# Optimization experiments

Hardware: AMD Instinct MI355X
Metric: run time of the kernel (lower is better)

The kernel has to match this reference:

```python
import jax, jax.numpy as jnp
import numpy as np

N_AGENTS = 32
STATE_DIM = 2048
EMBED = 64
BS, T = 64, 32


def setup_inputs() -> dict:
    key = jax.random.key(0)
    ks = jax.random.split(key, 12)
    def lin(k, fan_in, fan_out):
        return jax.random.normal(k, (fan_in, fan_out), dtype=jnp.float32) / np.sqrt(fan_in)
    return {
        "agent_qs": jax.random.normal(ks[0], (BS, T, N_AGENTS), dtype=jnp.float32),
        "states": jax.random.normal(ks[1], (BS, T, STATE_DIM), dtype=jnp.float32),
        "Ww1": lin(ks[2], STATE_DIM, EMBED * N_AGENTS),
        "bw1": jnp.zeros((EMBED * N_AGENTS,), jnp.float32),
        "Wwf": lin(ks[3], STATE_DIM, EMBED),
        "bwf": jnp.zeros((EMBED,), jnp.float32),
        "Wb1": lin(ks[4], STATE_DIM, EMBED),
        "bb1": jnp.zeros((EMBED,), jnp.float32),
        "Wv1": lin(ks[5], STATE_DIM, EMBED),
        "bv1": jnp.zeros((EMBED,), jnp.float32),
        "Wv2": lin(ks[6], EMBED, 1),
        "bv2": jnp.zeros((1,), jnp.float32),
    }


def _mix(qs, st, Ww1, bw1, Wwf, bwf, Wb1, bb1, Wv1, bv1, Wv2, bv2):
    # qs: [B,1,A], st: [B,S] -> q_tot [B]
    w1 = jnp.abs(st @ Ww1 + bw1).reshape(-1, N_AGENTS, EMBED)          # [B,A,E]
    b1 = (st @ Wb1 + bb1)[:, None, :]                                   # [B,1,E]
    hidden = jax.nn.elu(jnp.einsum('bia,bae->bie', qs, w1) + b1)        # [B,1,E]
    w_final = jnp.abs(st @ Wwf + bwf)                                   # [B,E]
    v = jax.nn.relu(st @ Wv1 + bv1) @ Wv2 + bv2                         # [B,1]
    y = jnp.einsum('bie,be->bi', hidden, w_final) + v                   # [B,1]
    return y[:, 0]


def reference(agent_qs, states, Ww1, bw1, Wwf, bwf, Wb1, bb1, Wv1, bv1, Wv2, bv2):
    bs = agent_qs.shape[0]
    st = states.reshape(-1, STATE_DIM)                   # [B,S]
    qs = agent_qs.reshape(-1, 1, N_AGENTS)               # [B,1,A]
    B = st.shape[0]
    params = (Ww1, bw1, Wwf, bwf, Wb1, bb1, Wv1, bv1, Wv2, bv2)

    # --- wc_calculate (fully detached) ---
    q_tot = _mix(qs, st, *params)                        # [B]
    dim2 = STATE_DIM // N_AGENTS
    st3 = st.reshape(B, N_AGENTS, dim2)
    mask = 1.0 - jnp.eye(N_AGENTS, dtype=st.dtype)       # [A,A]: row i zeros agent-i chunk
    masked = (st3[None, :, :, :] * mask[:, None, :, None]).reshape(N_AGENTS * B, STATE_DIM)
    qs_rep = jnp.broadcast_to(qs[None], (N_AGENTS, B, 1, N_AGENTS)).reshape(N_AGENTS * B, 1, N_AGENTS)
    q1 = _mix(qs_rep, masked, *params).reshape(N_AGENTS, B)
    wc = jnp.abs(q_tot[None, :] - q1).T                  # [B,A]
    wc = wc / jnp.maximum(jnp.linalg.norm(wc, axis=1, keepdims=True), 1e-12)
    wc = jax.lax.stop_gradient(wc)[:, None, :]           # [B,1,A]

    # --- final mix with importance-weighted qs ---
    q_tot_final = _mix(qs * wc, st, *params)             # [B]
    return q_tot_final.reshape(bs, -1, 1)
```

## Files before the change

kernel.cpp:

```cpp
#include <hip/hip_runtime.h>
#include <math.h>
#include <stdint.h>

#define NA 32
#define SD 2048
#define BT 2048
#define NFRG 144

typedef float floatx4 __attribute__((ext_vector_type(4)));
typedef short bf16x8  __attribute__((ext_vector_type(8)));

__device__ __forceinline__ unsigned short f2bf(float f) {
    union { float f; uint32_t u; } v; v.f = f;
    uint32_t r = v.u + 0x7FFFu + ((v.u >> 16) & 1u);
    return (unsigned short)(r >> 16);
}


__global__ __launch_bounds__(256) void k0_ast(const float* __restrict__ st,
                                              unsigned short* __restrict__ stA) {
    const int t  = threadIdx.x;
    const int kc = blockIdx.x * 4 + (t >> 6);
    const int bt = blockIdx.y;
    const int l  = t & 63;
    const int quad = l >> 4, l16 = l & 15;
    const float* src = st + (size_t)(bt * 16 + l16) * SD + kc * 32 + quad * 8;
    float4 v0 = *(const float4*)(src);
    float4 v1 = *(const float4*)(src + 4);
    ushort4 o0, o1;
    o0.x = f2bf(v0.x); o0.y = f2bf(v0.y); o0.z = f2bf(v0.z); o0.w = f2bf(v0.w);
    o1.x = f2bf(v1.x); o1.y = f2bf(v1.y); o1.z = f2bf(v1.z); o1.w = f2bf(v1.w);
    unsigned short* dst = stA + ((size_t)bt * 64 + kc) * 512 + l * 8;
    *(ushort4*)(dst)     = o0;
    *(ushort4*)(dst + 4) = o1;
}

__global__ __launch_bounds__(256) void k0_wswz(const float* __restrict__ Ww1,
                                               const float* __restrict__ Wwf,
                                               const float* __restrict__ Wb1,
                                               const float* __restrict__ Wv1,
                                               unsigned short* __restrict__ Wswz) {
    const int t = threadIdx.x;
    const int i = blockIdx.y;
    const int f = blockIdx.x * 2 + (t >> 7);
    const int h = (t >> 6) & 1;
    const int l = t & 63;
    const int quad = l >> 4, l16 = l & 15;
    const int n = f * 16 + l16;

    const float* src; int ld, nr = 0;
    if (f < 128)      { src = Ww1; ld = 2048; nr = n; }
    else if (f < 132) { src = Wwf; ld = 64;   nr = n - 2048; }
    else if (f < 136) { src = Wb1; ld = 64;   nr = n - 2112; }
    else if (f < 140) { src = Wv1; ld = 64;   nr = n - 2176; }
    else              { src = nullptr; ld = 64; }

    const int k0 = i * 64 + h * 32 + quad * 8;
    unsigned short vals[8];
    #pragma unroll
    for (int j = 0; j < 8; j++)
        vals[j] = src ? f2bf(src[(size_t)(k0 + j) * ld + nr]) : (unsigned short)0;

    unsigned short* dst = Wswz + (((size_t)i * NFRG + f) * 2 + h) * 512 + l * 8;
    ushort4 o0 = {vals[0], vals[1], vals[2], vals[3]};
    ushort4 o1 = {vals[4], vals[5], vals[6], vals[7]};
    *(ushort4*)(dst)     = o0;
    *(ushort4*)(dst + 4) = o1;
}

__global__ void k0_bias(const float* __restrict__ bw1, const float* __restrict__ bwf,
                        const float* __restrict__ bb1, const float* __restrict__ bv1,
                        float* __restrict__ bcat) {
    int n = blockIdx.x * 256 + threadIdx.x;
    if (n >= NFRG * 16) return;
    float v = 0.f;
    if (n < 2048)      v = bw1[n];
    else if (n < 2112) v = bwf[n - 2048];
    else if (n < 2176) v = bb1[n - 2112];
    else if (n < 2240) v = bv1[n - 2176];
    bcat[n] = v;
}

__global__ __launch_bounds__(256) void k1_gemm(const unsigned short* __restrict__ stA,
                                               const unsigned short* __restrict__ Wswz,
                                               const float* __restrict__ bcat,
                                               float* __restrict__ Ycn)
{
    const int t = threadIdx.x;
    const int m0t = blockIdx.x * 4;
    const int n0f = blockIdx.y * 8;
    const int wid = t >> 6, lane = t & 63;
    const int wm = wid & 1, wn = wid >> 1;
    const int l16 = lane & 15;

    floatx4 acc[2][4];
    #pragma unroll
    for (int i = 0; i < 2; i++)
        #pragma unroll
        for (int j = 0; j < 4; j++) acc[i][j] = (floatx4)0.f;

    const unsigned short* Ap0 = stA + ((size_t)(m0t + wm * 2 + 0) * 64) * 512 + lane * 8;
    const unsigned short* Ap1 = stA + ((size_t)(m0t + wm * 2 + 1) * 64) * 512 + lane * 8;
    const unsigned short* Bbase = Wswz + ((size_t)(n0f + wn * 4) * 2) * 512 + lane * 8;

    bf16x8 a0c = *(const bf16x8*)(Ap0);
    bf16x8 a1c = *(const bf16x8*)(Ap1);
    bf16x8 bc[4];
    #pragma unroll
    for (int nf = 0; nf < 4; nf++)
        bc[nf] = *(const bf16x8*)(Bbase + (size_t)nf * 1024);

    for (int kc = 0; kc < 64; kc++) {
        bf16x8 a0n, a1n, bn[4];
        if (kc < 63) {
            const int kn = kc + 1;
            a0n = *(const bf16x8*)(Ap0 + (size_t)kn * 512);
            a1n = *(const bf16x8*)(Ap1 + (size_t)kn * 512);
            const unsigned short* Bp =
                Bbase + ((size_t)(kn >> 1) * NFRG * 2 + (kn & 1)) * 512;
            #pragma unroll
            for (int nf = 0; nf < 4; nf++)
                bn[nf] = *(const bf16x8*)(Bp + (size_t)nf * 1024);
        }
        #pragma unroll
        for (int nf = 0; nf < 4; nf++) {
            acc[0][nf] = __builtin_amdgcn_mfma_f32_16x16x32_bf16(a0c, bc[nf], acc[0][nf], 0, 0, 0);
            acc[1][nf] = __builtin_amdgcn_mfma_f32_16x16x32_bf16(a1c, bc[nf], acc[1][nf], 0, 0, 0);
        }
        a0c = a0n; a1c = a1n;
        #pragma unroll
        for (int nf = 0; nf < 4; nf++) bc[nf] = bn[nf];
    }

    #pragma unroll
    for (int mf = 0; mf < 2; mf++)
        #pragma unroll
        for (int nf = 0; nf < 4; nf++) {
            const int f  = n0f + wn * 4 + nf;
            const int bt = m0t + wm * 2 + mf;
            const float bias = bcat[f * 16 + l16];
            floatx4 o;
            #pragma unroll
            for (int r = 0; r < 4; r++) o[r] = -(acc[mf][nf][r] + bias);
            *(floatx4*)(Ycn + ((size_t)bt * NFRG + f) * 256 + lane * 4) = o;
        }
}

__global__ __launch_bounds__(64) void k3_q1(
    const unsigned short* __restrict__ stA, const float* __restrict__ qs,
    const unsigned short* __restrict__ Wswz, const float* __restrict__ Wv2,
    const float* __restrict__ bv2, const float* __restrict__ Ycn,
    float* __restrict__ q1)
{
    const int i  = blockIdx.x;
    const int bt = blockIdx.y;
    __shared__ float qs_s[16][33];

    const int t = threadIdx.x;
    const int quad = t >> 4, l16 = t & 15;

    {
        int b = t >> 2, a0 = (t & 3) * 8;
        const float* src = qs + (size_t)(bt * 16 + b) * NA + a0;
        #pragma unroll
        for (int u = 0; u < 8; u++) qs_s[b][a0 + u] = src[u];
    }
    bf16x8 A0 = *(const bf16x8*)(stA + ((size_t)bt * 64 + 2 * i + 0) * 512 + t * 8);
    bf16x8 A1 = *(const bf16x8*)(stA + ((size_t)bt * 64 + 2 * i + 1) * 512 + t * 8);
    __syncthreads();

    floatx4 hid[4];
    #pragma unroll
    for (int nf = 0; nf < 4; nf++) hid[nf] = (floatx4)0.f;

    const float*          Yb = Ycn  + (size_t)bt * NFRG * 256;
    const unsigned short* Wb = Wswz + (size_t)i * NFRG * 1024;

    bf16x8 wc_[8];
    {
        const unsigned short* wp = Wb + t * 8;
        #pragma unroll
        for (int nf = 0; nf < 4; nf++) {
            wc_[nf * 2 + 0] = *(const bf16x8*)(wp + (size_t)nf * 1024);
            wc_[nf * 2 + 1] = *(const bf16x8*)(wp + (size_t)nf * 1024 + 512);
        }
    }

    for (int a = 0; a < 32; a++) {
        bf16x8 wn_[8];
        if (a < 31) {
            const unsigned short* wp = Wb + (size_t)((a + 1) * 4) * 1024 + t * 8;
            #pragma unroll
            for (int nf = 0; nf < 4; nf++) {
                wn_[nf * 2 + 0] = *(const bf16x8*)(wp + (size_t)nf * 1024);
                wn_[nf * 2 + 1] = *(const bf16x8*)(wp + (size_t)nf * 1024 + 512);
            }
        }
        const float* yp = Yb + (size_t)(a * 4) * 256 + t * 4;
        floatx4 acc[4];
        #pragma unroll
        for (int nf = 0; nf < 4; nf++) acc[nf] = *(const floatx4*)(yp + nf * 256);
        #pragma unroll
        for (int nf = 0; nf < 4; nf++) {
            acc[nf] = __builtin_amdgcn_mfma_f32_16x16x32_bf16(A0, wc_[nf*2+0], acc[nf], 0, 0, 0);
            acc[nf] = __builtin_amdgcn_mfma_f32_16x16x32_bf16(A1, wc_[nf*2+1], acc[nf], 0, 0, 0);
        }
        float qv[4];
        #pragma unroll
        for (int r = 0; r < 4; r++) qv[r] = qs_s[quad * 4 + r][a];
        #pragma unroll
        for (int nf = 0; nf < 4; nf++)
            #pragma unroll
            for (int r = 0; r < 4; r++)
                hid[nf][r] += qv[r] * fabsf(acc[nf][r]);
        #pragma unroll
        for (int u = 0; u < 8; u++) wc_[u] = wn_[u];
    }

    floatx4 wff[4], b1f[4], vacc = (floatx4)0.f;
    #pragma unroll
    for (int nft = 0; nft < 12; nft++) {
        const int f = 128 + nft;
        floatx4 c = *(const floatx4*)(Yb + (size_t)f * 256 + t * 4);
        const unsigned short* wp = Wb + (size_t)f * 1024 + t * 8;
        c = __builtin_amdgcn_mfma_f32_16x16x32_bf16(A0, *(const bf16x8*)(wp),       c, 0, 0, 0);
        c = __builtin_amdgcn_mfma_f32_16x16x32_bf16(A1, *(const bf16x8*)(wp + 512), c, 0, 0, 0);
        if (nft < 4) {
            #pragma unroll
            for (int r = 0; r < 4; r++) wff[nft][r] = fabsf(c[r]);
        } else if (nft < 8) {
            #pragma unroll
            for (int r = 0; r < 4; r++) b1f[nft - 4][r] = -c[r];
        } else {
            float wv2 = Wv2[(nft - 8) * 16 + l16];
            #pragma unroll
            for (int r = 0; r < 4; r++) vacc[r] += fmaxf(-c[r], 0.f) * wv2;
        }
    }

    const float bv2v = bv2[0];
    #pragma unroll
    for (int r = 0; r < 4; r++) {
        float s = vacc[r];
        #pragma unroll
        for (int nf = 0; nf < 4; nf++) {
            float h = hid[nf][r] + b1f[nf][r];
            h = h > 0.f ? h : expm1f(h);
            s += h * wff[nf][r];
        }
        s += __shfl_xor(s, 1); s += __shfl_xor(s, 2);
        s += __shfl_xor(s, 4); s += __shfl_xor(s, 8);
        if (l16 == 0) q1[(size_t)i * BT + bt * 16 + quad * 4 + r] = s + bv2v;
    }
}

__global__ __launch_bounds__(256) void k4_final(
    const float* __restrict__ qs, const float* __restrict__ Ycn,
    const float* __restrict__ q1, const float* __restrict__ Wv2,
    const float* __restrict__ bv2, float* __restrict__ out)
{
    const int bt = blockIdx.x;
    __shared__ float qs_s[16][33];
    __shared__ float qw_s[16][33];
    __shared__ float hidp[4][16][64];
    __shared__ float wfb[16][64], b1b[16][64], vb[16][64];
    __shared__ float qt[16];

    const int t = threadIdx.x, w = t >> 6, lane = t & 63;
    const int quad = lane >> 4, l16 = lane & 15;
    const float bv2v = bv2[0];

    {
        int l = t * 2;
        float2 v = *(const float2*)&qs[(size_t)(bt * 16 + (l >> 5)) * NA + (l & 31)];
        qs_s[l >> 5][(l & 31) + 0] = v.x;
        qs_s[l >> 5][(l & 31) + 1] = v.y;
    }
    __syncthreads();

    const float* Yb = Ycn + (size_t)bt * NFRG * 256;

    floatx4 hid[4];
    #pragma unroll
    for (int nf = 0; nf < 4; nf++) hid[nf] = (floatx4)0.f;
    for (int ia = 0; ia < 8; ia++) {
        const int a = w * 8 + ia;
        const float* yp = Yb + (size_t)(a * 4) * 256 + lane * 4;
        float qv[4];
        #pragma unroll
        for (int r = 0; r < 4; r++) qv[r] = qs_s[quad * 4 + r][a];
        #pragma unroll
        for (int nf = 0; nf < 4; nf++) {
            floatx4 c = *(const floatx4*)(yp + nf * 256);
            #pragma unroll
            for (int r = 0; r < 4; r++) hid[nf][r] += qv[r] * fabsf(c[r]);
        }
    }
    #pragma unroll
    for (int nf = 0; nf < 4; nf++)
        #pragma unroll
        for (int r = 0; r < 4; r++)
            hidp[w][quad * 4 + r][nf * 16 + l16] = hid[nf][r];

    #pragma unroll
    for (int fi = 0; fi < 3; fi++) {
        const int nft = w * 3 + fi;
        floatx4 c = *(const floatx4*)(Yb + (size_t)(128 + nft) * 256 + lane * 4);
        const int e = (nft & 3) * 16 + l16;
        #pragma unroll
        for (int r = 0; r < 4; r++) {
            int b = quad * 4 + r;
            if (nft < 4)      wfb[b][e] = fabsf(c[r]);
            else if (nft < 8) b1b[b][e] = -c[r];
            else              vb[b][e]  = fmaxf(-c[r], 0.f) * Wv2[e];
        }
    }
    __syncthreads();

    #pragma unroll
    for (int bb = 0; bb < 4; bb++) {
        int b = w * 4 + bb;
        float h = hidp[0][b][lane] + hidp[1][b][lane]
                + hidp[2][b][lane] + hidp[3][b][lane] + b1b[b][lane];
        h = h > 0.f ? h : expm1f(h);
        float val = h * wfb[b][lane] + vb[b][lane];
        #pragma unroll
        for (int off = 32; off > 0; off >>= 1) val += __shfl_xor(val, off);
        if (lane == 0) qt[b] = val + bv2v;
    }
    __syncthreads();

    {
        const int rr = w * 4 + quad;
        float qtv = qt[rr];
        float d0 = fabsf(qtv - q1[(size_t)(2 * l16 + 0) * BT + bt * 16 + rr]);
        float d1 = fabsf(qtv - q1[(size_t)(2 * l16 + 1) * BT + bt * 16 + rr]);
        float ss = d0 * d0 + d1 * d1;
        ss += __shfl_xor(ss, 1); ss += __shfl_xor(ss, 2);
        ss += __shfl_xor(ss, 4); ss += __shfl_xor(ss, 8);
        float inv = 1.f / fmaxf(sqrtf(ss), 1e-12f);
        qw_s[rr][2 * l16 + 0] = qs_s[rr][2 * l16 + 0] * d0 * inv;
        qw_s[rr][2 * l16 + 1] = qs_s[rr][2 * l16 + 1] * d1 * inv;
    }
    __syncthreads();

    floatx4 hid2[4];
    #pragma unroll
    for (int nf = 0; nf < 4; nf++) hid2[nf] = (floatx4)0.f;
    for (int ia = 0; ia < 8; ia++) {
        const int a = w * 8 + ia;
        const float* yp = Yb + (size_t)(a * 4) * 256 + lane * 4;
        float qv[4];
        #pragma unroll
        for (int r = 0; r < 4; r++) qv[r] = qw_s[quad * 4 + r][a];
        #pragma unroll
        for (int nf = 0; nf < 4; nf++) {
            floatx4 c = *(const floatx4*)(yp + nf * 256);
            #pragma unroll
            for (int r = 0; r < 4; r++) hid2[nf][r] += qv[r] * fabsf(c[r]);
        }
    }
    #pragma unroll
    for (int nf = 0; nf < 4; nf++)
        #pragma unroll
        for (int r = 0; r < 4; r++)
            hidp[w][quad * 4 + r][nf * 16 + l16] = hid2[nf][r];
    __syncthreads();

    #pragma unroll
    for (int bb = 0; bb < 4; bb++) {
        int b = w * 4 + bb;
        float h = hidp[0][b][lane] + hidp[1][b][lane]
                + hidp[2][b][lane] + hidp[3][b][lane] + b1b[b][lane];
        h = h > 0.f ? h : expm1f(h);
        float val = h * wfb[b][lane] + vb[b][lane];
        #pragma unroll
        for (int off = 32; off > 0; off >>= 1) val += __shfl_xor(val, off);
        if (lane == 0) out[bt * 16 + b] = val + bv2v;
    }
}

extern "C" void kernel_launch(void* const* d_in, const int* in_sizes, int n_in,
                              void* d_out, int out_size, void* d_ws, size_t ws_size,
                              hipStream_t stream) {
    const float* qs  = (const float*)d_in[0];
    const float* st  = (const float*)d_in[1];
    const float* Ww1 = (const float*)d_in[2];
    const float* bw1 = (const float*)d_in[3];
    const float* Wwf = (const float*)d_in[4];
    const float* bwf = (const float*)d_in[5];
    const float* Wb1 = (const float*)d_in[6];
    const float* bb1 = (const float*)d_in[7];
    const float* Wv1 = (const float*)d_in[8];
    const float* bv1 = (const float*)d_in[9];
    const float* Wv2 = (const float*)d_in[10];
    const float* bv2 = (const float*)d_in[11];
    float* out = (float*)d_out;

    float* Ycn           = (float*)d_ws;
    unsigned short* stA  = (unsigned short*)(Ycn + (size_t)128 * NFRG * 256);
    unsigned short* Wswz = stA + (size_t)SD * SD;
    float* bcat          = (float*)(Wswz + (size_t)32 * NFRG * 1024);
    float* q1v           = bcat + NFRG * 16;

    k0_ast <<<dim3(16, 128), 256, 0, stream>>>(st, stA);
    k0_wswz<<<dim3(NFRG / 2, 32), 256, 0, stream>>>(Ww1, Wwf, Wb1, Wv1, Wswz);
    k0_bias<<<(NFRG * 16 + 255) / 256, 256, 0, stream>>>(bw1, bwf, bb1, bv1, bcat);

    k1_gemm<<<dim3(BT / 64, NFRG / 8), 256, 0, stream>>>(stA, Wswz, bcat, Ycn);
    k3_q1  <<<dim3(NA, BT / 16), 64, 0, stream>>>(stA, qs, Wswz, Wv2, bv2, Ycn, q1v);
    k4_final<<<BT / 16, 256, 0, stream>>>(qs, Ycn, q1v, Wv2, bv2, out);
}
```

Measured before the change: 215.4 us.

## Restructure q1 kernel: 4-wave blocks sharing LDS-staged weights, two agents per wave

The masked-agent correction kernel now runs 256-thread blocks. Each wave handles one 16-row batch tile and two masked agents (p and p+16), and the four waves share weight fragments that are double-buffered in LDS through global_load_lds. The Ycn bias fragments are loaded once per tile and reused across both agents. This cuts redundant global weight and Ycn traffic per MFMA and overlaps the next fragment's load with compute. In exchange it adds per-iteration block barriers and more register pressure from the doubled accumulators.

```diff
diff --git a/kernel.cpp b/kernel.cpp
--- a/kernel.cpp
+++ b/kernel.cpp
@@ -14,6 +14,13 @@
     union { float f; uint32_t u; } v; v.f = f;
     uint32_t r = v.u + 0x7FFFu + ((v.u >> 16) & 1u);
     return (unsigned short)(r >> 16);
+}
+
+__device__ __forceinline__ void stage16(const void* g, void* l) {
+    __builtin_amdgcn_global_load_lds(
+        (const __attribute__((address_space(1))) void*)g,
+        (__attribute__((address_space(3))) void*)l,
+        16, 0, 0);
 }
 
 
@@ -146,112 +153,171 @@
         }
 }
 
-__global__ __launch_bounds__(64) void k3_q1(
+__global__ __launch_bounds__(256) void k3_q1(
     const unsigned short* __restrict__ stA, const float* __restrict__ qs,
     const unsigned short* __restrict__ Wswz, const float* __restrict__ Wv2,
     const float* __restrict__ bv2, const float* __restrict__ Ycn,
     float* __restrict__ q1)
 {
-    const int i  = blockIdx.x;
-    const int bt = blockIdx.y;
-    __shared__ float qs_s[16][33];
-
+    const int p   = blockIdx.x;
+    const int btg = blockIdx.y;
     const int t = threadIdx.x;
-    const int quad = t >> 4, l16 = t & 15;
-
-    {
-        int b = t >> 2, a0 = (t & 3) * 8;
+    const int w = t >> 6, lane = t & 63;
+    const int bt = btg * 4 + w;
+    const int quad = lane >> 4, l16 = lane & 15;
+    const int im[2] = { p, p + 16 };
+
+    __shared__ unsigned short Wl[2][2][4][2][512];
+    __shared__ float qs_s[4][16][33];
+
+    {
+        int b = lane >> 2, a0 = (lane & 3) * 8;
         const float* src = qs + (size_t)(bt * 16 + b) * NA + a0;
         #pragma unroll
-        for (int u = 0; u < 8; u++) qs_s[b][a0 + u] = src[u];
-    }
-    bf16x8 A0 = *(const bf16x8*)(stA + ((size_t)bt * 64 + 2 * i + 0) * 512 + t * 8);
-    bf16x8 A1 = *(const bf16x8*)(stA + ((size_t)bt * 64 + 2 * i + 1) * 512 + t * 8);
-    __syncthreads();
-
-    floatx4 hid[4];
-    #pragma unroll
-    for (int nf = 0; nf < 4; nf++) hid[nf] = (floatx4)0.f;
-
-    const float*          Yb = Ycn  + (size_t)bt * NFRG * 256;
-    const unsigned short* Wb = Wswz + (size_t)i * NFRG * 1024;
-
-    bf16x8 wc_[8];
-    {
-        const unsigned short* wp = Wb + t * 8;
-        #pragma unroll
-        for (int nf = 0; nf < 4; nf++) {
-            wc_[nf * 2 + 0] = *(const bf16x8*)(wp + (size_t)nf * 1024);
-            wc_[nf * 2 + 1] = *(const bf16x8*)(wp + (size_t)nf * 1024 + 512);
-        }
-    }
-
-    for (int a = 0; a < 32; a++) {
-        bf16x8 wn_[8];
-        if (a < 31) {
-            const unsigned short* wp = Wb + (size_t)((a + 1) * 4) * 1024 + t * 8;
+        for (int u = 0; u < 8; u++) qs_s[w][b][a0 + u] = src[u];
+    }
+
+    bf16x8 A0[2], A1[2];
+    #pragma unroll
+    for (int m = 0; m < 2; m++) {
+        A0[m] = *(const bf16x8*)(stA + ((size_t)bt * 64 + 2 * im[m] + 0) * 512 + lane * 8);
+        A1[m] = *(const bf16x8*)(stA + ((size_t)bt * 64 + 2 * im[m] + 1) * 512 + lane * 8);
+    }
+
+    const float* Yb = Ycn + (size_t)bt * NFRG * 256 + lane * 4;
+
+    auto stage = [&](int fg, int buf) {
+        #pragma unroll
+        for (int j = 0; j < 4; j++) {
+            const int c  = w * 4 + j;
+            const int m  = c >> 3;
+            const int nf = (c >> 1) & 3;
+            const int h  = c & 1;
+            const unsigned short* g = Wswz
+                + ((size_t)(im[m] * NFRG + fg * 4 + nf) * 2 + h) * 512 + lane * 8;
+            stage16(g, &Wl[buf][m][nf][h][0]);
+        }
+    };
+
+    floatx4 yv[4], yn[4], acc[2][4];
+
+    auto wmfma = [&](int buf) {
+        #pragma unroll
+        for (int m = 0; m < 2; m++)
             #pragma unroll
             for (int nf = 0; nf < 4; nf++) {
-                wn_[nf * 2 + 0] = *(const bf16x8*)(wp + (size_t)nf * 1024);
-                wn_[nf * 2 + 1] = *(const bf16x8*)(wp + (size_t)nf * 1024 + 512);
+                bf16x8 w0 = *(const bf16x8*)&Wl[buf][m][nf][0][lane * 8];
+                bf16x8 w1 = *(const bf16x8*)&Wl[buf][m][nf][1][lane * 8];
+                floatx4 a = __builtin_amdgcn_mfma_f32_16x16x32_bf16(A0[m], w0, yv[nf], 0, 0, 0);
+                acc[m][nf] = __builtin_amdgcn_mfma_f32_16x16x32_bf16(A1[m], w1, a, 0, 0, 0);
             }
-        }
-        const float* yp = Yb + (size_t)(a * 4) * 256 + t * 4;
-        floatx4 acc[4];
-        #pragma unroll
-        for (int nf = 0; nf < 4; nf++) acc[nf] = *(const floatx4*)(yp + nf * 256);
-        #pragma unroll
-        for (int nf = 0; nf < 4; nf++) {
-            acc[nf] = __builtin_amdgcn_mfma_f32_16x16x32_bf16(A0, wc_[nf*2+0], acc[nf], 0, 0, 0);
-            acc[nf] = __builtin_amdgcn_mfma_f32_16x16x32_bf16(A1, wc_[nf*2+1], acc[nf], 0, 0, 0);
-        }
+    };
+
+    floatx4 hid[2][4];
+    #pragma unroll
+    for (int m = 0; m < 2; m++)
+        #pragma unroll
+        for (int nf = 0; nf < 4; nf++) hid[m][nf] = (floatx4)0.f;
+
+    stage(0, 0);
+    #pragma unroll
+    for (int nf = 0; nf < 4; nf++) yv[nf] = *(const floatx4*)(Yb + (size_t)nf * 256);
+    __syncthreads();
+
+    for (int fg = 0; fg < 32; fg++) {
+        const int cur = fg & 1;
+        stage(fg + 1, cur ^ 1);
+        {
+            const float* yp = Yb + (size_t)(fg + 1) * 4 * 256;
+            #pragma unroll
+            for (int nf = 0; nf < 4; nf++) yn[nf] = *(const floatx4*)(yp + (size_t)nf * 256);
+        }
+        wmfma(cur);
         float qv[4];
         #pragma unroll
-        for (int r = 0; r < 4; r++) qv[r] = qs_s[quad * 4 + r][a];
-        #pragma unroll
-        for (int nf = 0; nf < 4; nf++)
-            #pragma unroll
-            for (int r = 0; r < 4; r++)
-                hid[nf][r] += qv[r] * fabsf(acc[nf][r]);
-        #pragma unroll
-        for (int u = 0; u < 8; u++) wc_[u] = wn_[u];
-    }
-
-    floatx4 wff[4], b1f[4], vacc = (floatx4)0.f;
-    #pragma unroll
-    for (int nft = 0; nft < 12; nft++) {
-        const int f = 128 + nft;
-        floatx4 c = *(const floatx4*)(Yb + (size_t)f * 256 + t * 4);
-        const unsigned short* wp = Wb + (size_t)f * 1024 + t * 8;
-        c = __builtin_amdgcn_mfma_f32_16x16x32_bf16(A0, *(const bf16x8*)(wp),       c, 0, 0, 0);
-        c = __builtin_amdgcn_mfma_f32_16x16x32_bf16(A1, *(const bf16x8*)(wp + 512), c, 0, 0, 0);
-        if (nft < 4) {
-            #pragma unroll
-            for (int r = 0; r < 4; r++) wff[nft][r] = fabsf(c[r]);
-        } else if (nft < 8) {
-            #pragma unroll
-            for (int r = 0; r < 4; r++) b1f[nft - 4][r] = -c[r];
-        } else {
-            float wv2 = Wv2[(nft - 8) * 16 + l16];
-            #pragma unroll
-            for (int r = 0; r < 4; r++) vacc[r] += fmaxf(-c[r], 0.f) * wv2;
+        for (int r = 0; r < 4; r++) qv[r] = qs_s[w][quad * 4 + r][fg];
+        #pragma unroll
+        for (int m = 0; m < 2; m++)
+            #pragma unroll
+            for (int nf = 0; nf < 4; nf++)
+                #pragma unroll
+                for (int r = 0; r < 4; r++)
+                    hid[m][nf][r] += qv[r] * fabsf(acc[m][nf][r]);
+        #pragma unroll
+        for (int nf = 0; nf < 4; nf++) yv[nf] = yn[nf];
+        __syncthreads();
+    }
+
+    floatx4 wff[2][4], b1f[2][4], vacc[2];
+
+    {
+        stage(33, 1);
+        {
+            const float* yp = Yb + (size_t)33 * 4 * 256;
+            #pragma unroll
+            for (int nf = 0; nf < 4; nf++) yn[nf] = *(const floatx4*)(yp + (size_t)nf * 256);
+        }
+        wmfma(0);
+        #pragma unroll
+        for (int m = 0; m < 2; m++)
+            #pragma unroll
+            for (int nf = 0; nf < 4; nf++)
+                #pragma unroll
+                for (int r = 0; r < 4; r++) wff[m][nf][r] = fabsf(acc[m][nf][r]);
+        #pragma unroll
+        for (int nf = 0; nf < 4; nf++) yv[nf] = yn[nf];
+        __syncthreads();
+    }
+    {
+        stage(34, 0);
+        {
+            const float* yp = Yb + (size_t)34 * 4 * 256;
+            #pragma unroll
+            for (int nf = 0; nf < 4; nf++) yn[nf] = *(const floatx4*)(yp + (size_t)nf * 256);
+        }
+        wmfma(1);
+        #pragma unroll
+        for (int m = 0; m < 2; m++)
+            #pragma unroll
+            for (int nf = 0; nf < 4; nf++)
+                #pragma unroll
+                for (int r = 0; r < 4; r++) b1f[m][nf][r] = -acc[m][nf][r];
+        #pragma unroll
+        for (int nf = 0; nf < 4; nf++) yv[nf] = yn[nf];
+        __syncthreads();
+    }
+    {
+        wmfma(0);
+        float wv2f[4];
+        #pragma unroll
+        for (int nf = 0; nf < 4; nf++) wv2f[nf] = Wv2[nf * 16 + l16];
+        #pragma unroll
+        for (int m = 0; m < 2; m++) {
+            vacc[m] = (floatx4)0.f;
+            #pragma unroll
+            for (int nf = 0; nf < 4; nf++)
+                #pragma unroll
+                for (int r = 0; r < 4; r++)
+                    vacc[m][r] += fmaxf(-acc[m][nf][r], 0.f) * wv2f[nf];
         }
     }
 
     const float bv2v = bv2[0];
     #pragma unroll
-    for (int r = 0; r < 4; r++) {
-        float s = vacc[r];
-        #pragma unroll
-        for (int nf = 0; nf < 4; nf++) {
-            float h = hid[nf][r] + b1f[nf][r];
-            h = h > 0.f ? h : expm1f(h);
-            s += h * wff[nf][r];
-        }
-        s += __shfl_xor(s, 1); s += __shfl_xor(s, 2);
-        s += __shfl_xor(s, 4); s += __shfl_xor(s, 8);
-        if (l16 == 0) q1[(size_t)i * BT + bt * 16 + quad * 4 + r] = s + bv2v;
-    }
+    for (int m = 0; m < 2; m++)
+        #pragma unroll
+        for (int r = 0; r < 4; r++) {
+            float s = vacc[m][r];
+            #pragma unroll
+            for (int nf = 0; nf < 4; nf++) {
+                float h = hid[m][nf][r] + b1f[m][nf][r];
+                h = h > 0.f ? h : expm1f(h);
+                s += h * wff[m][nf][r];
+            }
+            s += __shfl_xor(s, 1); s += __shfl_xor(s, 2);
+            s += __shfl_xor(s, 4); s += __shfl_xor(s, 8);
+            if (l16 == 0) q1[(size_t)im[m] * BT + bt * 16 + quad * 4 + r] = s + bv2v;
+        }
 }
 
 __global__ __launch_bounds__(256) void k4_final(
@@ -408,6 +474,6 @@
     k0_bias<<<(NFRG * 16 + 255) / 256, 256, 0, stream>>>(bw1, bwf, bb1, bv1, bcat);
 
     k1_gemm<<<dim3(BT / 64, NFRG / 8), 256, 0, stream>>>(stA, Wswz, bcat, Ycn);
-    k3_q1  <<<dim3(NA, BT / 16), 64, 0, stream>>>(stA, qs, Wswz, Wv2, bv2, Ycn, q1v);
+    k3_q1  <<<dim3(16, 32), 256, 0, stream>>>(stA, qs, Wswz, Wv2, bv2, Ycn, q1v);
     k4_final<<<BT / 16, 256, 0, stream>>>(qs, Ycn, q1v, Wv2, bv2, out);
 }
```

After: 193.3 us. -10.2%, faster.
